# Kernel tuning notes

Measured on AMD Instinct MI355X. Metric: run time of the kernel, lower is better.

Reference implementation:

```python
import jax, jax.numpy as jnp
import numpy as np

B, S, DIM = 64, 256, 512   # batch, seq, feature dim
Q, K = 8, 1024             # num_quantizers, codebook_size


def setup_inputs() -> dict:
    key = jax.random.key(0)
    kx, ke = jax.random.split(key)
    x = jax.random.normal(kx, (B, S, DIM), dtype=jnp.float32)
    # stacked per-quantizer codebooks (the torch module registers one embed buffer per layer)
    embeds = jax.random.normal(ke, (Q, K, DIM), dtype=jnp.float32)
    return {"x": x, "embeds": embeds}


def _residual_vq(x, embeds):
    shape = x.shape
    d = shape[-1]

    def step(carry, embed):
        residual, qout = carry
        flat = residual.reshape(-1, d)                       # [N, d]
        # squared euclidean distance to every code: [N, K]
        dist = (jnp.sum(flat * flat, axis=1, keepdims=True)
                + jnp.sum(embed * embed, axis=1)
                - 2.0 * flat @ embed.T)
        idx = jnp.argmin(dist, axis=1)                       # [N]
        q = embed[idx].reshape(shape)                        # gather == one-hot @ embed
        # commitment + embedding loss (mse with detach on opposite sides)
        commit = jnp.mean((jax.lax.stop_gradient(q) - residual) ** 2)
        embed_l = jnp.mean((q - jax.lax.stop_gradient(residual)) ** 2)
        # straight-through estimator
        q_st = residual + jax.lax.stop_gradient(q - residual)
        new_res = residual - jax.lax.stop_gradient(q_st)
        return (new_res, qout + q_st), (idx.reshape(shape[:-1]), commit + embed_l)

    (_, qout), (idxs, losses) = jax.lax.scan(step, (x, jnp.zeros_like(x)), embeds)
    indices = jnp.moveaxis(idxs, 0, -1)                      # (B, S, Q)
    return qout, indices, jnp.sum(losses)


def reference(x, embeds):
    return _residual_vq(x, embeds)
```

## Files before the change

kernel.cpp:

```cpp
#include <hip/hip_runtime.h>

#define NROWS   16384
#define DIM     512
#define QQ      8
#define KK      1024
#define QOUT_SZ (NROWS * DIM)
#define IDX_SZ  (NROWS * QQ)
#define BK      64

#define FLAG_REL 0.04f
#define FLAG_ABS 0.02f

#define RCH    32
#define RCODES (KK / RCH)

typedef __attribute__((ext_vector_type(8))) short short8x;
typedef __attribute__((ext_vector_type(4))) float f32x4;

typedef __attribute__((address_space(3))) uint32_t lds_u32;
typedef __attribute__((address_space(1))) const uint32_t ga_u32;
#define GLOBAL_LOAD_LDS16(g, l) \
    __builtin_amdgcn_global_load_lds((ga_u32*)(g), (lds_u32*)(l), 16, 0, 0)

#define WS_LOSSP_OFF 0
#define WS_LOSSR_OFF (1024 * 8)
#define WS_NFLAG_OFF (WS_LOSSR_OFF + 16)
#define WS_FLAG_OFF  (WS_NFLAG_OFF + 16)
#define WS_RNORM_OFF (WS_FLAG_OFF + NROWS * 4)
#define WS_ENORM_OFF (WS_RNORM_OFF + NROWS * 4)
#define WS_PD1_OFF   (WS_ENORM_OFF + QQ * KK * 4)
#define WS_PK1_OFF   (WS_PD1_OFF + 4 * NROWS * 4)
#define WS_PD2_OFF   (WS_PK1_OFF + 4 * NROWS * 4)
#define WS_PK2_OFF   (WS_PD2_OFF + 4 * NROWS * 4)
#define WS_PD3_OFF   (WS_PK2_OFF + 4 * NROWS * 4)
#define WS_EH_OFF    (WS_PD3_OFF + 4 * NROWS * 4)
#define WS_XH_OFF    (WS_EH_OFF + (size_t)QQ * KK * DIM * 2)
#define WS_RES_OFF   (WS_XH_OFF + (size_t)NROWS * DIM * 2)
#define WS_PACK_OFF  (WS_RES_OFF + (size_t)NROWS * DIM * 4)

__device__ inline unsigned short bf16rne(float f) {
    unsigned int u = __float_as_uint(f);
    return (unsigned short)((u + 0x7FFFu + ((u >> 16) & 1u)) >> 16);
}

__device__ inline void merge3(float& d1, int& k1, float& d2, int& k2, float& d3,
                              float o1, int q1, float o2, int q2, float o3) {
    bool bf = (o1 < d1) || (o1 == d1 && q1 < k1);
    float n1d, n2d, n3d; int n1k, n2k;
    if (bf) {
        n1d = o1; n1k = q1;
        bool b2 = (o2 < d1) || (o2 == d1 && q2 < k1);
        if (b2) { n2d = o2; n2k = q2; n3d = fminf(o3, d1); }
        else    { n2d = d1; n2k = k1; n3d = fminf(o2, d2); }
    } else {
        n1d = d1; n1k = k1;
        bool a2 = (d2 < o1) || (d2 == o1 && k2 < q1);
        if (a2) { n2d = d2; n2k = k2; n3d = fminf(d3, o1); }
        else    { n2d = o1; n2k = q1; n3d = fminf(d2, o2); }
    }
    d1 = n1d; k1 = n1k; d2 = n2d; k2 = n2k; d3 = n3d;
}

__global__ __launch_bounds__(256) void k_enorm(const float4* __restrict__ e4,
                                               float* __restrict__ enorm) {
    int row  = blockIdx.x * 4 + (threadIdx.x >> 6);
    int lane = threadIdx.x & 63;
    float s = 0.f;
#pragma unroll
    for (int i = 0; i < 2; i++) {
        int c = lane + i * 64;
        float4 v = e4[row * (DIM / 4) + c];
        s += v.x * v.x + v.y * v.y + v.z * v.z + v.w * v.w;
    }
#pragma unroll
    for (int off = 32; off; off >>= 1) s += __shfl_down(s, off, 64);
    if (lane == 0) enorm[row] = s;
}

__global__ __launch_bounds__(256) void k_prep(const float4* __restrict__ x4,
                                              float4* __restrict__ res4,
                                              float* __restrict__ rnorm,
                                              unsigned short* __restrict__ Xh,
                                              double* __restrict__ loss_rare) {
    if (blockIdx.x == 0 && threadIdx.x == 0) *loss_rare = 0.0;
    int row  = blockIdx.x * 4 + (threadIdx.x >> 6);
    int lane = threadIdx.x & 63;
    float s = 0.f;
#pragma unroll
    for (int i = 0; i < 2; i++) {
        int c = lane + i * 64;
        float4 v = x4[row * (DIM / 4) + c];
        res4[row * (DIM / 4) + c] = v;
        *(ushort4*)&Xh[(size_t)row * DIM + c * 4] =
            make_ushort4(bf16rne(v.x), bf16rne(v.y), bf16rne(v.z), bf16rne(v.w));
        s += v.x * v.x + v.y * v.y + v.z * v.z + v.w * v.w;
    }
#pragma unroll
    for (int off = 32; off; off >>= 1) s += __shfl_down(s, off, 64);
    if (lane == 0) rnorm[row] = s;
}

__global__ __launch_bounds__(256) void k_ecast(const float4* __restrict__ e4,
                                               unsigned short* __restrict__ EhAll) {
    int i = blockIdx.x * 256 + threadIdx.x;
    float4 v = e4[i];
    *(ushort4*)&EhAll[(size_t)i * 4] =
        make_ushort4(bf16rne(v.x), bf16rne(v.y), bf16rne(v.z), bf16rne(v.w));
}

__global__ __launch_bounds__(512, 4) void k_gemm(
        const unsigned short* __restrict__ Xh,
        const unsigned short* __restrict__ Eh,
        const float* __restrict__ enorm_q,
        float* __restrict__ pd1, int* __restrict__ pk1,
        float* __restrict__ pd2, int* __restrict__ pk2,
        float* __restrict__ pd3, int* __restrict__ nflag) {
    __shared__ __align__(16) unsigned short sXh[128 * BK];
    __shared__ __align__(16) unsigned short sEh[256 * BK];
    __shared__ float sD1[2][128]; __shared__ int sK1[2][128];
    __shared__ float sD2[2][128]; __shared__ int sK2[2][128];
    __shared__ float sD3[2][128];

    const int tid = threadIdx.x;
    if (blockIdx.x == 0 && tid == 0) *nflag = 0;
    const int l   = tid & 63;
    const int w   = tid >> 6;
    const int wm  = w >> 1;
    const int wn  = w & 1;
    const int xcd = blockIdx.x & 7;
    const int tt  = blockIdx.x >> 3;
    const int nt  = tt & 3;
    const int mt  = ((tt >> 2) << 3) | xcd;
    const int l15 = l & 15;
    const int lq4 = l >> 4;
    const int srow = l >> 3;
    const int sgrp = (l & 7) ^ srow;

    f32x4 acc[2][8];
#pragma unroll
    for (int rt = 0; rt < 2; rt++)
#pragma unroll
        for (int ct = 0; ct < 8; ct++) acc[rt][ct] = (f32x4){0.f, 0.f, 0.f, 0.f};

    const unsigned short* gX = Xh + (size_t)(mt * 128) * DIM;
    const unsigned short* gE = Eh + (size_t)(nt * 256) * DIM;
    const int swz = l15 & 7;

    for (int c = 0; c < 8; c++) {
        __syncthreads();
#pragma unroll
        for (int i = 0; i < 2; i++) {
            int r = w * 16 + i * 8 + srow;
            GLOBAL_LOAD_LDS16(gX + (size_t)r * DIM + c * BK + sgrp * 8,
                              &sXh[(w * 16 + i * 8) * BK]);
        }
#pragma unroll
        for (int i = 0; i < 4; i++) {
            int r = w * 32 + i * 8 + srow;
            GLOBAL_LOAD_LDS16(gE + (size_t)r * DIM + c * BK + sgrp * 8,
                              &sEh[(w * 32 + i * 8) * BK]);
        }
        __syncthreads();

#pragma unroll
        for (int ks = 0; ks < 2; ks++) {
            const int g = ((ks * 4 + lq4) ^ swz) * 8;
            const int r0 = wm * 32 + l15;
            short8x a0 = *(const short8x*)&sXh[r0 * BK + g];
            short8x a1 = *(const short8x*)&sXh[(r0 + 16) * BK + g];
#pragma unroll
            for (int ct = 0; ct < 8; ct++) {
                const int br = wn * 128 + ct * 16 + l15;
                short8x b = *(const short8x*)&sEh[br * BK + g];
                acc[0][ct] = __builtin_amdgcn_mfma_f32_16x16x32_bf16(a0, b, acc[0][ct], 0, 0, 0);
                acc[1][ct] = __builtin_amdgcn_mfma_f32_16x16x32_bf16(a1, b, acc[1][ct], 0, 0, 0);
            }
        }
    }

    float d1[2][4], d2[2][4], d3[2][4]; int k1[2][4], k2[2][4];
#pragma unroll
    for (int rt = 0; rt < 2; rt++)
#pragma unroll
        for (int r = 0; r < 4; r++) {
            d1[rt][r] = 3.4e38f; d2[rt][r] = 3.4e38f; d3[rt][r] = 3.4e38f;
            k1[rt][r] = 0; k2[rt][r] = 0;
        }

#pragma unroll
    for (int ct = 0; ct < 8; ct++) {
        int codeg = nt * 256 + wn * 128 + ct * 16 + l15;
        float en = enorm_q[codeg];
#pragma unroll
        for (int rt = 0; rt < 2; rt++)
#pragma unroll
            for (int r = 0; r < 4; r++) {
                float d = en - 2.0f * acc[rt][ct][r];
                bool b1 = d < d1[rt][r];
                bool b2 = d < d2[rt][r];
                bool b3 = d < d3[rt][r];
                d3[rt][r] = b2 ? d2[rt][r] : (b3 ? d : d3[rt][r]);
                d2[rt][r] = b1 ? d1[rt][r] : (b2 ? d : d2[rt][r]);
                k2[rt][r] = b1 ? k1[rt][r] : (b2 ? codeg : k2[rt][r]);
                d1[rt][r] = b1 ? d : d1[rt][r];
                k1[rt][r] = b1 ? codeg : k1[rt][r];
            }
    }
#pragma unroll
    for (int m = 1; m < 16; m <<= 1) {
#pragma unroll
        for (int rt = 0; rt < 2; rt++)
#pragma unroll
            for (int r = 0; r < 4; r++) {
                float o1 = __shfl_xor(d1[rt][r], m, 64);
                int   q1 = __shfl_xor(k1[rt][r], m, 64);
                float o2 = __shfl_xor(d2[rt][r], m, 64);
                int   q2 = __shfl_xor(k2[rt][r], m, 64);
                float o3 = __shfl_xor(d3[rt][r], m, 64);
                merge3(d1[rt][r], k1[rt][r], d2[rt][r], k2[rt][r], d3[rt][r],
                       o1, q1, o2, q2, o3);
            }
    }
    if (l15 == 0) {
#pragma unroll
        for (int rt = 0; rt < 2; rt++)
#pragma unroll
            for (int r = 0; r < 4; r++) {
                int rloc = wm * 32 + rt * 16 + lq4 * 4 + r;
                sD1[wn][rloc] = d1[rt][r]; sK1[wn][rloc] = k1[rt][r];
                sD2[wn][rloc] = d2[rt][r]; sK2[wn][rloc] = k2[rt][r];
                sD3[wn][rloc] = d3[rt][r];
            }
    }
    __syncthreads();
    if (tid < 128) {
        float a1 = sD1[0][tid], a2 = sD2[0][tid], a3 = sD3[0][tid];
        int   ak1 = sK1[0][tid], ak2 = sK2[0][tid];
        merge3(a1, ak1, a2, ak2, a3,
               sD1[1][tid], sK1[1][tid], sD2[1][tid], sK2[1][tid], sD3[1][tid]);
        int grow = mt * 128 + tid;
        pd1[nt * NROWS + grow] = a1; pk1[nt * NROWS + grow] = ak1;
        pd2[nt * NROWS + grow] = a2; pk2[nt * NROWS + grow] = ak2;
        pd3[nt * NROWS + grow] = a3;
    }
}

__global__ __launch_bounds__(512) void k_post(
        const float* __restrict__ pd1, const int* __restrict__ pk1,
        const float* __restrict__ pd2, const int* __restrict__ pk2,
        const float* __restrict__ pd3,
        float* __restrict__ res, float* __restrict__ rnorm,
        unsigned short* __restrict__ Xh,
        const float* __restrict__ embed_q, const float* __restrict__ enorm_q,
        double* __restrict__ loss_part, float* __restrict__ out_idx,
        int* __restrict__ nflag, int* __restrict__ flag_list,
        unsigned long long* __restrict__ packed, int q) {
    __shared__ int sIdx1[16], sIdx2[16], sFlag[16], sFast[16];
    __shared__ float ls_loss[8];

    const int tid = threadIdx.x;
    const int rbase = blockIdx.x * 16;

    if (tid < 16) {
        int row = rbase + tid;
        float d1 = pd1[row], d2 = pd2[row], d3 = pd3[row];
        int   k1 = pk1[row], k2 = pk2[row];
#pragma unroll
        for (int nt = 1; nt < 4; nt++) {
            merge3(d1, k1, d2, k2, d3,
                   pd1[nt * NROWS + row], pk1[nt * NROWS + row],
                   pd2[nt * NROWS + row], pk2[nt * NROWS + row],
                   pd3[nt * NROWS + row]);
        }
        sIdx1[tid] = k1; sIdx2[tid] = k2;
        float thr = FLAG_REL * sqrtf(rnorm[row]) + FLAG_ABS;
        int fl = (d3 - d1) < thr;
        sFlag[tid] = fl;
        sFast[tid] = (d2 - d1) >= thr;
        if (fl) {
            int p = atomicAdd(nflag, 1);
            flag_list[p] = row;
            packed[p] = 0xFFFFFFFFFFFFFFFFull;
        }
    }
    __syncthreads();

    {
        const int rloc = tid >> 5, seg = tid & 31;
        const int row  = rbase + rloc;
        const int k1   = sIdx1[rloc], k2 = sIdx2[rloc];
        const int fl   = sFlag[rloc];
        const int fast = sFast[rloc];
        const int wave = tid >> 6, lid = tid & 63;
        const float4* r4 = (const float4*)res + (size_t)row * (DIM / 4);
        const float4* a4 = (const float4*)embed_q + (size_t)k1 * (DIM / 4);
        float4 rv[4], av[4];
#pragma unroll
        for (int u = 0; u < 4; u++) {
            rv[u] = r4[seg + 32 * u];
            av[u] = a4[seg + 32 * u];
        }
        int kw = k1;
        if (!fast) {
            const float4* b4 = (const float4*)embed_q + (size_t)k2 * (DIM / 4);
            float4 bv[4];
            float dot1 = 0.f, dot2 = 0.f;
#pragma unroll
            for (int u = 0; u < 4; u++) {
                bv[u] = b4[seg + 32 * u];
                dot1 += rv[u].x * av[u].x; dot1 += rv[u].y * av[u].y;
                dot1 += rv[u].z * av[u].z; dot1 += rv[u].w * av[u].w;
                dot2 += rv[u].x * bv[u].x; dot2 += rv[u].y * bv[u].y;
                dot2 += rv[u].z * bv[u].z; dot2 += rv[u].w * bv[u].w;
            }
#pragma unroll
            for (int m = 1; m < 32; m <<= 1) {
                dot1 += __shfl_xor(dot1, m, 64);
                dot2 += __shfl_xor(dot2, m, 64);
            }
            float rn = rnorm[row];
            float da = (rn + enorm_q[k1]) - 2.0f * dot1;
            float db = (rn + enorm_q[k2]) - 2.0f * dot2;
            bool useb = (db < da || (db == da && k2 < k1));
            if (useb) {
                kw = k2;
#pragma unroll
                for (int u = 0; u < 4; u++) av[u] = bv[u];
            }
        }

        float sl = 0.f;
        if (!fl) {
            float sr = 0.f;
#pragma unroll
            for (int u = 0; u < 4; u++) {
                float4 ev = av[u];
                float tx = ev.x - rv[u].x, ty = ev.y - rv[u].y;
                float tz = ev.z - rv[u].z, tw = ev.w - rv[u].w;
                float qx = rv[u].x + tx, qy = rv[u].y + ty;
                float qz = rv[u].z + tz, qw = rv[u].w + tw;
                float nx = rv[u].x - qx, ny = rv[u].y - qy;
                float nz = rv[u].z - qz, nw = rv[u].w - qw;
                int col = seg + 32 * u;
                ((float4*)res)[(size_t)row * (DIM / 4) + col] =
                    make_float4(nx, ny, nz, nw);
                *(ushort4*)&Xh[(size_t)row * DIM + col * 4] =
                    make_ushort4(bf16rne(nx), bf16rne(ny), bf16rne(nz), bf16rne(nw));
                sl += tx * tx + ty * ty + tz * tz + tw * tw;
                sr += nx * nx + ny * ny + nz * nz + nw * nw;
            }
            if (seg == 0) out_idx[(size_t)row * QQ + q] = (float)kw;
            float srr = sr;
#pragma unroll
            for (int m = 1; m < 32; m <<= 1) srr += __shfl_xor(srr, m, 64);
            if (seg == 0) rnorm[row] = srr;
        }
#pragma unroll
        for (int m = 1; m < 64; m <<= 1) sl += __shfl_xor(sl, m, 64);
        if (lid == 0) ls_loss[wave] = sl;
    }
    __syncthreads();
    if (tid == 0) {
        float s = 0.f;
#pragma unroll
        for (int w = 0; w < 8; w++) s += ls_loss[w];
        double cur = (q == 0) ? 0.0 : loss_part[blockIdx.x];
        loss_part[blockIdx.x] = cur + (double)s;
    }
}

__global__ __launch_bounds__(256) void k_rare1(
        const int* __restrict__ nflag, const int* __restrict__ flag_list,
        const float* __restrict__ res, const float* __restrict__ rnorm,
        const float* __restrict__ embed_q, const float* __restrict__ enorm_q,
        unsigned long long* __restrict__ packed) {
    __shared__ unsigned long long swmin[4];
    const int nf = *nflag;
    const int tid  = threadIdx.x;
    const int c    = blockIdx.x & (RCH - 1);
    const int fs   = blockIdx.x >> 5;
    const int fstp = (int)(gridDim.x >> 5);
    const int code = c * RCODES + (tid >> 3);
    const int seg  = tid & 7;
    const int lane = tid & 63, wv = tid >> 6;
    const float* ep = embed_q + (size_t)code * DIM + seg * 64;
    const float  en = enorm_q[code];
    for (int f = fs; f < nf; f += fstp) {
        const int row = flag_list[f];
        const float* rp = res + (size_t)row * DIM + seg * 64;
        float dot = 0.f;
#pragma unroll
        for (int u = 0; u < 16; u++) {
            float4 r = *(const float4*)(rp + u * 4);
            float4 e = *(const float4*)(ep + u * 4);
            dot += r.x * e.x; dot += r.y * e.y;
            dot += r.z * e.z; dot += r.w * e.w;
        }
#pragma unroll
        for (int m = 1; m < 8; m <<= 1) dot += __shfl_xor(dot, m, 64);
        unsigned long long pk = 0xFFFFFFFFFFFFFFFFull;
        if (seg == 0) {
            float dist = (rnorm[row] + en) - 2.0f * dot;
            unsigned int u = __float_as_uint(dist);
            u = (u & 0x80000000u) ? ~u : (u | 0x80000000u);
            pk = ((unsigned long long)u << 32) | (unsigned int)code;
        }
#pragma unroll
        for (int m = 8; m < 64; m <<= 1) {
            unsigned int hi = (unsigned int)(pk >> 32), lo = (unsigned int)pk;
            unsigned int ohi = (unsigned int)__shfl_xor((int)hi, m, 64);
            unsigned int olo = (unsigned int)__shfl_xor((int)lo, m, 64);
            unsigned long long o = ((unsigned long long)ohi << 32) | olo;
            if (o < pk) pk = o;
        }
        if (lane == 0) swmin[wv] = pk;
        __syncthreads();
        if (tid == 0) {
            unsigned long long b = swmin[0];
            if (swmin[1] < b) b = swmin[1];
            if (swmin[2] < b) b = swmin[2];
            if (swmin[3] < b) b = swmin[3];
            atomicMin(&packed[f], b);
        }
        __syncthreads();
    }
}

__global__ __launch_bounds__(128) void k_rare2(
        const int* __restrict__ nflag, const int* __restrict__ flag_list,
        const unsigned long long* __restrict__ packed,
        float* __restrict__ res, float* __restrict__ rnorm,
        unsigned short* __restrict__ Xh,
        const float* __restrict__ embed_q,
        double* __restrict__ loss_rare, float* __restrict__ out_idx, int q) {
    __shared__ float ls[2], rs[2];
    const int nf = *nflag;
    const int tid = threadIdx.x;
    const int lid = tid & 63, wv = tid >> 6;
    for (int f = blockIdx.x; f < nf; f += gridDim.x) {
        const int row   = flag_list[f];
        const int kbest = (int)(packed[f] & 0xFFFFFFFFull);
        float4 rv = *(const float4*)&res[(size_t)row * DIM + tid * 4];
        float4 ev = *(const float4*)&embed_q[(size_t)kbest * DIM + tid * 4];
        float tx = ev.x - rv.x, ty = ev.y - rv.y, tz = ev.z - rv.z, tw = ev.w - rv.w;
        float qx = rv.x + tx, qy = rv.y + ty, qz = rv.z + tz, qw = rv.w + tw;
        float nx = rv.x - qx, ny = rv.y - qy, nz = rv.z - qz, nw = rv.w - qw;
        *(float4*)&res[(size_t)row * DIM + tid * 4] = make_float4(nx, ny, nz, nw);
        *(ushort4*)&Xh[(size_t)row * DIM + tid * 4] =
            make_ushort4(bf16rne(nx), bf16rne(ny), bf16rne(nz), bf16rne(nw));
        float sl = tx * tx + ty * ty + tz * tz + tw * tw;
        float sr = nx * nx + ny * ny + nz * nz + nw * nw;
#pragma unroll
        for (int m = 1; m < 64; m <<= 1) {
            sl += __shfl_xor(sl, m, 64);
            sr += __shfl_xor(sr, m, 64);
        }
        if (lid == 0) { ls[wv] = sl; rs[wv] = sr; }
        __syncthreads();
        if (tid == 0) {
            rnorm[row] = rs[0] + rs[1];
            atomicAdd(loss_rare, (double)(ls[0] + ls[1]));
            out_idx[(size_t)row * QQ + q] = (float)kbest;
        }
        __syncthreads();
    }
}

__global__ __launch_bounds__(256) void k_final(const float4* __restrict__ x4,
                                               const float4* __restrict__ res4,
                                               float4* __restrict__ out4,
                                               const double* __restrict__ loss_part,
                                               const double* __restrict__ loss_rare,
                                               float* __restrict__ out_scalar) {
    int i = blockIdx.x * 256 + threadIdx.x;
    float4 a = x4[i], b = res4[i];
    out4[i] = make_float4(a.x - b.x, a.y - b.y, a.z - b.z, a.w - b.w);
    if (blockIdx.x == 0 && threadIdx.x < 64) {
        double s = 0.0;
#pragma unroll
        for (int j = 0; j < 16; j++) s += loss_part[threadIdx.x + 64 * j];
#pragma unroll
        for (int m = 1; m < 64; m <<= 1) s += __shfl_xor(s, m, 64);
        if (threadIdx.x == 0)
            out_scalar[0] = (float)((s + *loss_rare) * 2.0 / (double)QOUT_SZ);
    }
}

extern "C" void kernel_launch(void* const* d_in, const int* in_sizes, int n_in,
                              void* d_out, int out_size, void* d_ws, size_t ws_size,
                              hipStream_t stream) {
    const float* x      = (const float*)d_in[0];
    const float* embeds = (const float*)d_in[1];

    char*   ws        = (char*)d_ws;
    double* loss_part = (double*)(ws + WS_LOSSP_OFF);
    double* loss_rare = (double*)(ws + WS_LOSSR_OFF);
    int*    nflag     = (int*)   (ws + WS_NFLAG_OFF);
    int*    flag_list = (int*)   (ws + WS_FLAG_OFF);
    float*  rnorm     = (float*) (ws + WS_RNORM_OFF);
    float*  enorm     = (float*) (ws + WS_ENORM_OFF);
    float*  pd1       = (float*) (ws + WS_PD1_OFF);
    int*    pk1       = (int*)   (ws + WS_PK1_OFF);
    float*  pd2       = (float*) (ws + WS_PD2_OFF);
    int*    pk2       = (int*)   (ws + WS_PK2_OFF);
    float*  pd3       = (float*) (ws + WS_PD3_OFF);
    unsigned short* EhAll = (unsigned short*)(ws + WS_EH_OFF);
    unsigned short* Xh    = (unsigned short*)(ws + WS_XH_OFF);
    float*  res       = (float*) (ws + WS_RES_OFF);
    unsigned long long* packed = (unsigned long long*)(ws + WS_PACK_OFF);

    float* out_q      = (float*)d_out;
    float* out_idx    = out_q + QOUT_SZ;
    float* out_scalar = out_q + QOUT_SZ + IDX_SZ;

    k_enorm<<<(QQ * KK) / 4, 256, 0, stream>>>((const float4*)embeds, enorm);
    k_prep <<<NROWS / 4, 256, 0, stream>>>((const float4*)x, (float4*)res, rnorm, Xh, loss_rare);
    k_ecast<<<(QQ * KK * DIM) / 4 / 256, 256, 0, stream>>>((const float4*)embeds, EhAll);

    for (int q = 0; q < QQ; q++) {
        const float* embed_q = embeds + (size_t)q * KK * DIM;
        const float* enorm_q = enorm + q * KK;
        const unsigned short* Eh_q = EhAll + (size_t)q * KK * DIM;
        k_gemm<<<512, 512, 0, stream>>>(Xh, Eh_q, enorm_q, pd1, pk1, pd2, pk2, pd3, nflag);
        k_post<<<1024, 512, 0, stream>>>(pd1, pk1, pd2, pk2, pd3, res, rnorm, Xh,
                                         embed_q, enorm_q, loss_part, out_idx,
                                         nflag, flag_list, packed, q);
        k_rare1<<<1024, 256, 0, stream>>>(nflag, flag_list, res, rnorm,
                                          embed_q, enorm_q, packed);
        k_rare2<<<128, 128, 0, stream>>>(nflag, flag_list, packed, res, rnorm, Xh,
                                         embed_q, loss_rare, out_idx, q);
    }

    k_final<<<QOUT_SZ / 4 / 256, 256, 0, stream>>>((const float4*)x, (const float4*)res,
                                                   (float4*)d_out, loss_part, loss_rare,
                                                   out_scalar);
}
```

Baseline: 763.9 us.

## Double-buffer GEMM LDS tiles, splitting codebook tile into halves for load/compute overlap

```diff
diff --git a/kernel.cpp b/kernel.cpp
--- a/kernel.cpp
+++ b/kernel.cpp
@@ -115,8 +115,8 @@
         float* __restrict__ pd1, int* __restrict__ pk1,
         float* __restrict__ pd2, int* __restrict__ pk2,
         float* __restrict__ pd3, int* __restrict__ nflag) {
-    __shared__ __align__(16) unsigned short sXh[128 * BK];
-    __shared__ __align__(16) unsigned short sEh[256 * BK];
+    __shared__ __align__(16) unsigned short sXh[2][128 * BK];
+    __shared__ __align__(16) unsigned short sEh[2][128 * BK];
     __shared__ float sD1[2][128]; __shared__ int sK1[2][128];
     __shared__ float sD2[2][128]; __shared__ int sK2[2][128];
     __shared__ float sD3[2][128];
@@ -146,35 +146,55 @@
     const unsigned short* gE = Eh + (size_t)(nt * 256) * DIM;
     const int swz = l15 & 7;
 
-    for (int c = 0; c < 8; c++) {
-        __syncthreads();
+    auto STAGE_X = [&](int buf, int c) {
 #pragma unroll
         for (int i = 0; i < 2; i++) {
             int r = w * 16 + i * 8 + srow;
             GLOBAL_LOAD_LDS16(gX + (size_t)r * DIM + c * BK + sgrp * 8,
-                              &sXh[(w * 16 + i * 8) * BK]);
-        }
-#pragma unroll
-        for (int i = 0; i < 4; i++) {
-            int r = w * 32 + i * 8 + srow;
-            GLOBAL_LOAD_LDS16(gE + (size_t)r * DIM + c * BK + sgrp * 8,
-                              &sEh[(w * 32 + i * 8) * BK]);
-        }
-        __syncthreads();
-
-#pragma unroll
-        for (int ks = 0; ks < 2; ks++) {
-            const int g = ((ks * 4 + lq4) ^ swz) * 8;
-            const int r0 = wm * 32 + l15;
-            short8x a0 = *(const short8x*)&sXh[r0 * BK + g];
-            short8x a1 = *(const short8x*)&sXh[(r0 + 16) * BK + g];
-#pragma unroll
-            for (int ct = 0; ct < 8; ct++) {
-                const int br = wn * 128 + ct * 16 + l15;
-                short8x b = *(const short8x*)&sEh[br * BK + g];
-                acc[0][ct] = __builtin_amdgcn_mfma_f32_16x16x32_bf16(a0, b, acc[0][ct], 0, 0, 0);
-                acc[1][ct] = __builtin_amdgcn_mfma_f32_16x16x32_bf16(a1, b, acc[1][ct], 0, 0, 0);
-            }
+                              &sXh[buf][(w * 16 + i * 8) * BK]);
+        }
+    };
+    auto STAGE_E = [&](int buf, int c, int h) {
+#pragma unroll
+        for (int i = 0; i < 2; i++) {
+            int r = w * 16 + i * 8 + srow;
+            GLOBAL_LOAD_LDS16(gE + (size_t)(h * 128 + r) * DIM + c * BK + sgrp * 8,
+                              &sEh[buf][(w * 16 + i * 8) * BK]);
+        }
+    };
+
+    STAGE_X(0, 0);
+    STAGE_E(0, 0, 0);
+    __syncthreads();
+
+    for (int c = 0; c < 8; c++) {
+        const int bx = c & 1;
+#pragma unroll
+        for (int h = 0; h < 2; h++) {
+            const int be = h;
+            if (h == 0) {
+                STAGE_E(1, c, 1);
+            } else if (c < 7) {
+                STAGE_X(bx ^ 1, c + 1);
+                STAGE_E(0, c + 1, 0);
+            }
+#pragma unroll
+            for (int ks = 0; ks < 2; ks++) {
+                const int g = ((ks * 4 + lq4) ^ swz) * 8;
+                const int r0 = wm * 32 + l15;
+                short8x a0 = *(const short8x*)&sXh[bx][r0 * BK + g];
+                short8x a1 = *(const short8x*)&sXh[bx][(r0 + 16) * BK + g];
+#pragma unroll
+                for (int ct = 0; ct < 4; ct++) {
+                    const int br = wn * 64 + ct * 16 + l15;
+                    short8x b = *(const short8x*)&sEh[be][br * BK + g];
+                    acc[0][h * 4 + ct] =
+                        __builtin_amdgcn_mfma_f32_16x16x32_bf16(a0, b, acc[0][h * 4 + ct], 0, 0, 0);
+                    acc[1][h * 4 + ct] =
+                        __builtin_amdgcn_mfma_f32_16x16x32_bf16(a1, b, acc[1][h * 4 + ct], 0, 0, 0);
+                }
+            }
+            __syncthreads();
         }
     }
 
@@ -188,14 +208,14 @@
         }
 
 #pragma unroll
-    for (int ct = 0; ct < 8; ct++) {
-        int codeg = nt * 256 + wn * 128 + ct * 16 + l15;
+    for (int j = 0; j < 8; j++) {
+        int codeg = nt * 256 + (j >> 2) * 128 + wn * 64 + (j & 3) * 16 + l15;
         float en = enorm_q[codeg];
 #pragma unroll
         for (int rt = 0; rt < 2; rt++)
 #pragma unroll
             for (int r = 0; r < 4; r++) {
-                float d = en - 2.0f * acc[rt][ct][r];
+                float d = en - 2.0f * acc[rt][j][r];
                 bool b1 = d < d1[rt][r];
                 bool b2 = d < d2[rt][r];
                 bool b3 = d < d3[rt][r];
```

New measurement: 789.8 us. +3.4%, slower.

## Fuse rare-row rescoring and residual update via last-block-done counter

Applied to the files above, without the earlier changes.

```diff
diff --git a/kernel.cpp b/kernel.cpp
--- a/kernel.cpp
+++ b/kernel.cpp
@@ -37,6 +37,7 @@
 #define WS_XH_OFF    (WS_EH_OFF + (size_t)QQ * KK * DIM * 2)
 #define WS_RES_OFF   (WS_XH_OFF + (size_t)NROWS * DIM * 2)
 #define WS_PACK_OFF  (WS_RES_OFF + (size_t)NROWS * DIM * 4)
+#define WS_DONE_OFF  (WS_PACK_OFF + (size_t)NROWS * 8)
 
 __device__ inline unsigned short bf16rne(float f) {
     unsigned int u = __float_as_uint(f);
@@ -254,7 +255,8 @@
         const float* __restrict__ embed_q, const float* __restrict__ enorm_q,
         double* __restrict__ loss_part, float* __restrict__ out_idx,
         int* __restrict__ nflag, int* __restrict__ flag_list,
-        unsigned long long* __restrict__ packed, int q) {
+        unsigned long long* __restrict__ packed, unsigned int* __restrict__ done,
+        int q) {
     __shared__ int sIdx1[16], sIdx2[16], sFlag[16], sFast[16];
     __shared__ float ls_loss[8];
 
@@ -281,6 +283,7 @@
             int p = atomicAdd(nflag, 1);
             flag_list[p] = row;
             packed[p] = 0xFFFFFFFFFFFFFFFFull;
+            done[p]   = 0u;
         }
     }
     __syncthreads();
@@ -369,16 +372,20 @@
     }
 }
 
-__global__ __launch_bounds__(256) void k_rare1(
+__global__ __launch_bounds__(256) void k_rare(
         const int* __restrict__ nflag, const int* __restrict__ flag_list,
-        const float* __restrict__ res, const float* __restrict__ rnorm,
+        float* __restrict__ res, float* __restrict__ rnorm,
+        unsigned short* __restrict__ Xh,
         const float* __restrict__ embed_q, const float* __restrict__ enorm_q,
-        unsigned long long* __restrict__ packed) {
+        unsigned long long* __restrict__ packed, unsigned int* __restrict__ done,
+        double* __restrict__ loss_rare, float* __restrict__ out_idx, int q) {
     __shared__ unsigned long long swmin[4];
+    __shared__ int sLast, sBestK;
+    __shared__ float ls[4], rs[4];
     const int nf = *nflag;
     const int tid  = threadIdx.x;
     const int c    = blockIdx.x & (RCH - 1);
-    const int fs   = blockIdx.x >> 5;
+    const int fs   = (int)(blockIdx.x >> 5);
     const int fstp = (int)(gridDim.x >> 5);
     const int code = c * RCODES + (tid >> 3);
     const int seg  = tid & 7;
@@ -421,46 +428,44 @@
             if (swmin[2] < b) b = swmin[2];
             if (swmin[3] < b) b = swmin[3];
             atomicMin(&packed[f], b);
+            __threadfence();
+            unsigned int cnt = atomicAdd(&done[f], 1u);
+            int last = (cnt == (unsigned int)(RCH - 1));
+            sLast = last;
+            if (last) {
+                unsigned long long fin = atomicAdd(&packed[f], 0ull);
+                sBestK = (int)(fin & 0xFFFFFFFFull);
+            }
         }
         __syncthreads();
-    }
-}
-
-__global__ __launch_bounds__(128) void k_rare2(
-        const int* __restrict__ nflag, const int* __restrict__ flag_list,
-        const unsigned long long* __restrict__ packed,
-        float* __restrict__ res, float* __restrict__ rnorm,
-        unsigned short* __restrict__ Xh,
-        const float* __restrict__ embed_q,
-        double* __restrict__ loss_rare, float* __restrict__ out_idx, int q) {
-    __shared__ float ls[2], rs[2];
-    const int nf = *nflag;
-    const int tid = threadIdx.x;
-    const int lid = tid & 63, wv = tid >> 6;
-    for (int f = blockIdx.x; f < nf; f += gridDim.x) {
-        const int row   = flag_list[f];
-        const int kbest = (int)(packed[f] & 0xFFFFFFFFull);
-        float4 rv = *(const float4*)&res[(size_t)row * DIM + tid * 4];
-        float4 ev = *(const float4*)&embed_q[(size_t)kbest * DIM + tid * 4];
-        float tx = ev.x - rv.x, ty = ev.y - rv.y, tz = ev.z - rv.z, tw = ev.w - rv.w;
-        float qx = rv.x + tx, qy = rv.y + ty, qz = rv.z + tz, qw = rv.w + tw;
-        float nx = rv.x - qx, ny = rv.y - qy, nz = rv.z - qz, nw = rv.w - qw;
-        *(float4*)&res[(size_t)row * DIM + tid * 4] = make_float4(nx, ny, nz, nw);
-        *(ushort4*)&Xh[(size_t)row * DIM + tid * 4] =
-            make_ushort4(bf16rne(nx), bf16rne(ny), bf16rne(nz), bf16rne(nw));
-        float sl = tx * tx + ty * ty + tz * tz + tw * tw;
-        float sr = nx * nx + ny * ny + nz * nz + nw * nw;
-#pragma unroll
-        for (int m = 1; m < 64; m <<= 1) {
-            sl += __shfl_xor(sl, m, 64);
-            sr += __shfl_xor(sr, m, 64);
-        }
-        if (lid == 0) { ls[wv] = sl; rs[wv] = sr; }
-        __syncthreads();
-        if (tid == 0) {
-            rnorm[row] = rs[0] + rs[1];
-            atomicAdd(loss_rare, (double)(ls[0] + ls[1]));
-            out_idx[(size_t)row * QQ + q] = (float)kbest;
+        if (sLast) {
+            const int kbest = sBestK;
+            float sl = 0.f, sr = 0.f;
+            if (tid < 128) {
+                float4 rv = *(const float4*)&res[(size_t)row * DIM + tid * 4];
+                float4 ev = *(const float4*)&embed_q[(size_t)kbest * DIM + tid * 4];
+                float tx = ev.x - rv.x, ty = ev.y - rv.y;
+                float tz = ev.z - rv.z, tw = ev.w - rv.w;
+                float qx = rv.x + tx, qy = rv.y + ty, qz = rv.z + tz, qw = rv.w + tw;
+                float nx = rv.x - qx, ny = rv.y - qy, nz = rv.z - qz, nw = rv.w - qw;
+                *(float4*)&res[(size_t)row * DIM + tid * 4] = make_float4(nx, ny, nz, nw);
+                *(ushort4*)&Xh[(size_t)row * DIM + tid * 4] =
+                    make_ushort4(bf16rne(nx), bf16rne(ny), bf16rne(nz), bf16rne(nw));
+                sl = tx * tx + ty * ty + tz * tz + tw * tw;
+                sr = nx * nx + ny * ny + nz * nz + nw * nw;
+            }
+#pragma unroll
+            for (int m = 1; m < 64; m <<= 1) {
+                sl += __shfl_xor(sl, m, 64);
+                sr += __shfl_xor(sr, m, 64);
+            }
+            if (lane == 0) { ls[wv] = sl; rs[wv] = sr; }
+            __syncthreads();
+            if (tid == 0) {
+                rnorm[row] = rs[0] + rs[1] + rs[2] + rs[3];
+                atomicAdd(loss_rare, (double)(ls[0] + ls[1] + ls[2] + ls[3]));
+                out_idx[(size_t)row * QQ + q] = (float)kbest;
+            }
         }
         __syncthreads();
     }
@@ -508,6 +513,7 @@
     unsigned short* Xh    = (unsigned short*)(ws + WS_XH_OFF);
     float*  res       = (float*) (ws + WS_RES_OFF);
     unsigned long long* packed = (unsigned long long*)(ws + WS_PACK_OFF);
+    unsigned int* done = (unsigned int*)(ws + WS_DONE_OFF);
 
     float* out_q      = (float*)d_out;
     float* out_idx    = out_q + QOUT_SZ;
@@ -524,11 +530,10 @@
         k_gemm<<<512, 512, 0, stream>>>(Xh, Eh_q, enorm_q, pd1, pk1, pd2, pk2, pd3, nflag);
         k_post<<<1024, 512, 0, stream>>>(pd1, pk1, pd2, pk2, pd3, res, rnorm, Xh,
                                          embed_q, enorm_q, loss_part, out_idx,
-                                         nflag, flag_list, packed, q);
-        k_rare1<<<1024, 256, 0, stream>>>(nflag, flag_list, res, rnorm,
-                                          embed_q, enorm_q, packed);
-        k_rare2<<<128, 128, 0, stream>>>(nflag, flag_list, packed, res, rnorm, Xh,
-                                         embed_q, loss_rare, out_idx, q);
+                                         nflag, flag_list, packed, done, q);
+        k_rare<<<2048, 256, 0, stream>>>(nflag, flag_list, res, rnorm, Xh,
+                                         embed_q, enorm_q, packed, done,
+                                         loss_rare, out_idx, q);
     }
 
     k_final<<<QOUT_SZ / 4 / 256, 256, 0, stream>>>((const float4*)x, (const float4*)res,
```

Result: slower. 1.012 ms (+32.5%).
